# Kernel optimization log

Hardware: AMD Instinct MI355X
Metric: run time of the kernel (lower is better)

The kernel has to match this reference:

```python
import jax, jax.numpy as jnp
import numpy as np

N, B, T, D = 6, 4, 1024, 768
P = 3            # number of prior phases
H, Dh = 2, 32    # n_heads, head_dim
I = H * Dh       # inner_dim
EPS = 1e-5


def setup_inputs() -> dict:
    key = jax.random.key(0)
    ks = jax.random.split(key, 9)
    current_states = jax.random.normal(ks[0], (N, B, T, D), dtype=jnp.float32)
    history_states = jax.random.normal(ks[1], (P, N, B, T, D), dtype=jnp.float32)
    attention_mask = jax.random.randint(ks[2], (B, T), 0, 2, dtype=jnp.int32)
    # Linear weights stored as [in, out] (transposed nn.Linear weight)
    s = 1.0 / np.sqrt(D)
    Wq = jax.random.uniform(ks[3], (N, D, I), jnp.float32, -s, s)  # per-domain q proj
    Wk = jax.random.uniform(ks[4], (D, I), jnp.float32, -s, s)     # shared k proj
    Wv = jax.random.uniform(ks[5], (D, I), jnp.float32, -s, s)     # shared v proj
    so = 1.0 / np.sqrt(I)
    Wo = jax.random.uniform(ks[6], (N, I, D), jnp.float32, -so, so)  # per-domain out proj
    gamma = jnp.ones((N, D), jnp.float32)   # per-domain LayerNorm weight
    beta = jnp.zeros((N, D), jnp.float32)   # per-domain LayerNorm bias
    return {"current_states": current_states, "history_states": history_states,
            "attention_mask": attention_mask, "Wq": Wq, "Wk": Wk, "Wv": Wv,
            "Wo": Wo, "gamma": gamma, "beta": beta}


def reference(current_states, history_states, attention_mask, Wq, Wk, Wv, Wo, gamma, beta):
    x = current_states                                   # [N,B,T,D]
    # concat prior phases along time per domain: [N,B,P*T,D]
    prior = jnp.transpose(history_states, (1, 2, 0, 3, 4)).reshape(N, B, P * T, D)

    q = jnp.einsum('nbtd,ndi->nbti', x, Wq).reshape(N, B, T, H, Dh).transpose(0, 1, 3, 2, 4)       # [N,B,H,T,Dh]
    k = jnp.einsum('nbsd,di->nbsi', prior, Wk).reshape(N, B, P * T, H, Dh).transpose(0, 1, 3, 2, 4)  # [N,B,H,S,Dh]
    v = jnp.einsum('nbsd,di->nbsi', prior, Wv).reshape(N, B, P * T, H, Dh).transpose(0, 1, 3, 2, 4)

    scale = 1.0 / jnp.sqrt(jnp.float32(Dh))
    scores = jnp.einsum('nbhtd,nbhsd->nbhts', q, k) * scale  # [N,B,H,T,P*T]
    full_mask = jnp.tile(attention_mask.astype(jnp.float32), (1, P))  # [B,P*T]
    bias = (1.0 - full_mask)[None, :, None, None, :] * -10000.0
    attn = jax.nn.softmax(scores + bias, axis=-1)
    o = jnp.einsum('nbhts,nbhsd->nbhtd', attn, v)            # [N,B,H,T,Dh]
    o = o.transpose(0, 1, 3, 2, 4).reshape(N, B, T, I)       # [N,B,T,I]
    o = jnp.einsum('nbti,nid->nbtd', o, Wo)                  # [N,B,T,D]

    y = x + o  # residual (dropout p=0)
    mu = jnp.mean(y, axis=-1, keepdims=True)
    var = jnp.mean(jnp.square(y - mu), axis=-1, keepdims=True)
    out = (y - mu) * jax.lax.rsqrt(var + EPS)
    out = out * gamma[:, None, None, :] + beta[:, None, None, :]
    return out
```

## Files before the change

### kernel.cpp

```cpp
#include <hip/hip_runtime.h>
#include <hip/hip_bf16.h>
#include <math.h>

#define NDOM 6
#define BB 4
#define TT 1024
#define DD 768
#define PP 3
#define HH 2
#define DHH 32
#define II 64
#define SS (PP*TT)
#define NROW (NDOM*BB*TT)
#define NKVROW (NDOM*BB*SS)
#define NSPLIT 4
#define NKVB (NKVROW/128)
#define NQB  (NROW/128)
#define LNEPS 1e-5f

typedef unsigned int uint;
typedef uint  u32x4  __attribute__((ext_vector_type(4)));
typedef int   i32x2  __attribute__((ext_vector_type(2)));
typedef float f32x2  __attribute__((ext_vector_type(2)));
typedef float f32x4  __attribute__((ext_vector_type(4)));
typedef float f32x16 __attribute__((ext_vector_type(16)));
typedef __bf16 bf16x8 __attribute__((ext_vector_type(8)));

__device__ __forceinline__ f32x16 mfma32(u32x4 a, u32x4 b, f32x16 c) {
  return __builtin_amdgcn_mfma_f32_32x32x16_bf16(
      __builtin_bit_cast(bf16x8, a), __builtin_bit_cast(bf16x8, b), c, 0, 0, 0);
}

__device__ __forceinline__ uint pkbf(float a, float b) {
  union { __bf16 h[2]; uint u; } v;
  v.h[0] = (__bf16)a; v.h[1] = (__bf16)b;
  return v.u;
}
__device__ __forceinline__ float b2f(uint u16) {
  union { uint i; float f; } v; v.i = u16 << 16; return v.f;
}

__device__ __forceinline__ void plswap(uint a, uint b, uint& x, uint& y) {
#if __has_builtin(__builtin_amdgcn_permlane32_swap)
  i32x2 r = __builtin_amdgcn_permlane32_swap((int)a, (int)b, false, false);
  x = (uint)r.x; y = (uint)r.y;
#else
  uint sa = __shfl_xor(a, 32), sb = __shfl_xor(b, 32);
  bool h1 = (threadIdx.x & 32) != 0;
  x = h1 ? sb : a;
  y = h1 ? b : sa;
#endif
}

__global__ __launch_bounds__(256) void prep_kernel(
    const int* __restrict__ mask, const float* __restrict__ Wk,
    const float* __restrict__ Wv, const float* __restrict__ Wq,
    const float* __restrict__ Wo,
    __hip_bfloat16* __restrict__ Bkv, __hip_bfloat16* __restrict__ Bq,
    __hip_bfloat16* __restrict__ Bo, float* __restrict__ bias2)
{
  int i = blockIdx.x * 256 + threadIdx.x;
  const int N1 = 128 * 768;
  const int N2 = NDOM * 64 * 768;
  const int N3 = NDOM * 768 * 64;
  if (i < N1) {
    int c = i / 768, k = i % 768;
    float v = (c < 64) ? Wk[k * 64 + c] : Wv[k * 64 + (c - 64)];
    Bkv[i] = __float2bfloat16(v);
  } else if (i < N1 + N2) {
    int j = i - N1;
    int n = j / (64 * 768);
    int rem = j % (64 * 768);
    int c = rem / 768, k = rem % 768;
    Bq[j] = __float2bfloat16(Wq[((size_t)n * 768 + k) * 64 + c]);
  } else if (i < N1 + N2 + N3) {
    int j = i - N1 - N2;
    int n = j / (768 * 64);
    int rem = j % (768 * 64);
    int d = rem / 64, k = rem % 64;
    Bo[j] = __float2bfloat16(Wo[((size_t)n * 64 + k) * 768 + d]);
  } else if (i < N1 + N2 + N3 + BB * SS) {
    int j = i - N1 - N2 - N3;
    int b = j / SS, s = j % SS;
    bias2[j] = (1.0f - (float)mask[b * TT + (s & (TT - 1))]) * (-14426.950408889634f);
  }
}

__global__ __launch_bounds__(256) void qkv_gemm_kernel(
    const float* __restrict__ x, const float* __restrict__ hist,
    const __hip_bfloat16* __restrict__ Bkv, const __hip_bfloat16* __restrict__ Bq,
    __hip_bfloat16* __restrict__ Qo, __hip_bfloat16* __restrict__ Kh,
    __hip_bfloat16* __restrict__ Vt2)
{
  __shared__ uint As[2][128 * 32];
  const int tid = threadIdx.x;
  const int lane = tid & 63, w = tid >> 6;
  const int cl = lane & 31, hi = lane >> 5;
  const int r0 = tid >> 3, oct = tid & 7;

  const bool isKV = blockIdx.x < NKVB;
  const float* Asrc;
  int nb = 0, s0 = 0, n = 0, brow = 0;
  if (isKV) {
    brow = blockIdx.x * 128;
    nb = brow / SS; n = nb >> 2;
    int b = nb & 3;
    s0 = brow % SS;
    int p = s0 / TT, t0 = s0 % TT;
    Asrc = hist + (((size_t)(p * NDOM + n) * BB + b) * TT + t0) * 768;
  } else {
    brow = (blockIdx.x - NKVB) * 128;
    n = brow >> 12;
    Asrc = x + (size_t)brow * 768;
  }

  float4 a0[4], a1[4];
  auto ldA = [&](int kk) {
#pragma unroll
    for (int g = 0; g < 4; ++g) {
      const float* ap = Asrc + (size_t)(r0 + 32 * g) * 768 + kk * 64 + oct * 8;
      a0[g] = *(const float4*)ap;
      a1[g] = *(const float4*)(ap + 4);
    }
  };
  auto stA = [&](uint* dst) {
#pragma unroll
    for (int g = 0; g < 4; ++g) {
      int row = r0 + 32 * g;
      u32x4 pk = {pkbf(a0[g].x, a0[g].y), pkbf(a0[g].z, a0[g].w),
                  pkbf(a1[g].x, a1[g].y), pkbf(a1[g].z, a1[g].w)};
      *(u32x4*)&dst[row * 32 + ((oct ^ (row & 7)) << 2)] = pk;
    }
  };

  if (isKV) {
    f32x16 acc0 = {}, acc1 = {}, acc2 = {}, acc3 = {};
    ldA(0);
    for (int kk = 0; kk < 12; ++kk) {
      uint* dst = As[kk & 1];
      stA(dst);
      __syncthreads();
      if (kk + 1 < 12) ldA(kk + 1);
#pragma unroll
      for (int ks = 0; ks < 4; ++ks) {
        int kg = kk * 64 + ks * 16 + hi * 8;
        u32x4 b0 = *(const u32x4*)(Bkv + (size_t)(cl)      * 768 + kg);
        u32x4 b1 = *(const u32x4*)(Bkv + (size_t)(32 + cl) * 768 + kg);
        u32x4 b2 = *(const u32x4*)(Bkv + (size_t)(64 + cl) * 768 + kg);
        u32x4 b3 = *(const u32x4*)(Bkv + (size_t)(96 + cl) * 768 + kg);
        int ro = w * 32 + cl;
        int oc = ks * 2 + hi;
        u32x4 a = *(const u32x4*)&dst[ro * 32 + ((oc ^ (ro & 7)) << 2)];
        acc0 = mfma32(a, b0, acc0);
        acc1 = mfma32(a, b1, acc1);
        acc2 = mfma32(a, b2, acc2);
        acc3 = mfma32(a, b3, acc3);
      }
    }
    {
      const size_t base0 = (size_t)(nb * 2 + 0) * SS;
      const size_t base1 = (size_t)(nb * 2 + 1) * SS;
#pragma unroll
      for (int r = 0; r < 16; ++r) {
        int rl = (r & 3) + 8 * (r >> 2) + 4 * hi;
        int s  = s0 + w * 32 + rl;
        Kh[(base0 + s) * 32 + cl] = __float2bfloat16(acc0[r]);
        Kh[(base1 + s) * 32 + cl] = __float2bfloat16(acc1[r]);
      }
    }
#pragma unroll
    for (int k = 0; k < 4; ++k) {
      int sb = (s0 + w * 32 + 8 * k) >> 3;
      size_t A0 = (((size_t)(nb * 2 + 0) * (SS / 8) + sb) * 32 + cl) * 8 + 4 * hi;
      size_t A1 = (((size_t)(nb * 2 + 1) * (SS / 8) + sb) * 32 + cl) * 8 + 4 * hi;
      *(uint2*)(Vt2 + A0) = uint2{pkbf(acc2[4*k], acc2[4*k+1]), pkbf(acc2[4*k+2], acc2[4*k+3])};
      *(uint2*)(Vt2 + A1) = uint2{pkbf(acc3[4*k], acc3[4*k+1]), pkbf(acc3[4*k+2], acc3[4*k+3])};
    }
  } else {
    const __hip_bfloat16* Bn = Bq + (size_t)n * 64 * 768;
    f32x16 acc0 = {}, acc1 = {};
    ldA(0);
    for (int kk = 0; kk < 12; ++kk) {
      uint* dst = As[kk & 1];
      stA(dst);
      __syncthreads();
      if (kk + 1 < 12) ldA(kk + 1);
#pragma unroll
      for (int ks = 0; ks < 4; ++ks) {
        int kg = kk * 64 + ks * 16 + hi * 8;
        u32x4 b0 = *(const u32x4*)(Bn + (size_t)(cl)      * 768 + kg);
        u32x4 b1 = *(const u32x4*)(Bn + (size_t)(32 + cl) * 768 + kg);
        int ro = w * 32 + cl;
        int oc = ks * 2 + hi;
        u32x4 a = *(const u32x4*)&dst[ro * 32 + ((oc ^ (ro & 7)) << 2)];
        acc0 = mfma32(a, b0, acc0);
        acc1 = mfma32(a, b1, acc1);
      }
    }
#pragma unroll
    for (int r = 0; r < 16; ++r) {
      int rl = (r & 3) + 8 * (r >> 2) + 4 * hi;
      size_t rb = (size_t)(brow + w * 32 + rl) * 64;
      Qo[rb + cl]      = __float2bfloat16(acc0[r]);
      Qo[rb + 32 + cl] = __float2bfloat16(acc1[r]);
    }
  }
}

struct KV { u32x4 k0, k1, k2, k3, v0, v1, v2, v3; };

__global__ __launch_bounds__(256) void attn_kernel(
    const __hip_bfloat16* __restrict__ Q, const __hip_bfloat16* __restrict__ Kh,
    const __hip_bfloat16* __restrict__ Vt2, const float* __restrict__ bias2,
    __hip_bfloat16* __restrict__ Op, float* __restrict__ Mp, float* __restrict__ Lp)
{
  const int tid = threadIdx.x;
  const int lane = tid & 63, w = tid >> 6;
  const int cl = lane & 31, hi = lane >> 5;
  const int bid = blockIdx.x;
  const int g = bid % 48;
  const int rest = bid / 48;
  const int sp = rest >> 3;
  const int tq = rest & 7;
  const int qtile = tq * 4 + w;
  const int h = g & 1, nb = g >> 1;
  const int b = nb & 3;
  const int qrow = nb * TT + qtile * 32;
  const int sbase = sp * (SS / NSPLIT);

  const __hip_bfloat16* Qp = Q + (size_t)(qrow + cl) * 64 + h * 32 + hi * 8;
  u32x4 qf0 = *(const u32x4*)Qp;
  u32x4 qf1 = *(const u32x4*)(Qp + 16);

  const __hip_bfloat16* Kp = Kh + ((size_t)(nb * 2 + h) * SS + sbase) * 32;
  const __hip_bfloat16* Vp = Vt2 + (size_t)(nb * 2 + h) * SS * 32 + (size_t)sbase * 32;
  const float* Bp = bias2 + b * SS + sbase + hi * 4;

  const float scale2 = 0.17677669529663687f * 1.4426950408889634f;
  const f32x2 sc2 = {scale2, scale2};

  f32x16 ot = {};
  float m = -1e30f, lsum = 0.f;

  auto loadKV = [&](int it) {
    KV t;
    const __hip_bfloat16* kp = Kp + (size_t)it * 64 * 32;
    t.k0 = *(const u32x4*)(kp + cl * 32 + hi * 8);
    t.k1 = *(const u32x4*)(kp + cl * 32 + 16 + hi * 8);
    t.k2 = *(const u32x4*)(kp + 1024 + cl * 32 + hi * 8);
    t.k3 = *(const u32x4*)(kp + 1024 + cl * 32 + 16 + hi * 8);
    const __hip_bfloat16* vp = Vp + (size_t)it * 64 * 32;
    t.v0 = *(const u32x4*)(vp + ((0 * 2 + hi) * 32 + cl) * 8);
    t.v1 = *(const u32x4*)(vp + ((1 * 2 + hi) * 32 + cl) * 8);
    t.v2 = *(const u32x4*)(vp + ((2 * 2 + hi) * 32 + cl) * 8);
    t.v3 = *(const u32x4*)(vp + ((3 * 2 + hi) * 32 + cl) * 8);
    return t;
  };

  auto compute = [&](const KV& t, int it) {
    f32x16 pz0 = {}, pz1 = {};
    pz0 = mfma32(t.k0, qf0, pz0);
    pz0 = mfma32(t.k1, qf1, pz0);
    pz1 = mfma32(t.k2, qf0, pz1);
    pz1 = mfma32(t.k3, qf1, pz1);
    const float* bp = Bp + it * 64;
    f32x4 b4[8];
#pragma unroll
    for (int q = 0; q < 8; ++q) b4[q] = *(const f32x4*)(bp + 8 * q);
    f32x2 p2[16];
#pragma unroll
    for (int i = 0; i < 8; ++i) {
      f32x4 bq0 = b4[i >> 1];
      f32x4 bq1 = b4[4 + (i >> 1)];
      f32x2 bv0 = (i & 1) ? f32x2{bq0.z, bq0.w} : f32x2{bq0.x, bq0.y};
      f32x2 bv1 = (i & 1) ? f32x2{bq1.z, bq1.w} : f32x2{bq1.x, bq1.y};
      p2[i]     = f32x2{pz0[2*i], pz0[2*i+1]} * sc2 + bv0;
      p2[8 + i] = f32x2{pz1[2*i], pz1[2*i+1]} * sc2 + bv1;
    }
    f32x2 mx = p2[0];
#pragma unroll
    for (int i = 1; i < 16; ++i) {
      mx.x = fmaxf(mx.x, p2[i].x);
      mx.y = fmaxf(mx.y, p2[i].y);
    }
    float tm = fmaxf(mx.x, mx.y);
    tm = fmaxf(tm, __shfl_xor(tm, 32));
    if (!__all(tm - m <= 8.f)) {
      float mn = fmaxf(m, tm);
      float f = exp2f(m - mn);
#pragma unroll
      for (int i = 0; i < 16; ++i) ot[i] *= f;
      lsum *= f;
      m = mn;
    }
    const f32x2 m2 = {m, m};
    f32x2 s2 = {0.f, 0.f};
#pragma unroll
    for (int i = 0; i < 16; ++i) {
      f32x2 d = p2[i] - m2;
      f32x2 e = {exp2f(d.x), exp2f(d.y)};
      p2[i] = e;
      s2 += e;
    }
    float ts = s2.x + s2.y;
    ts += __shfl_xor(ts, 32);
    lsum += ts;
    uint cv[16];
#pragma unroll
    for (int i = 0; i < 16; ++i) cv[i] = pkbf(p2[i].x, p2[i].y);
    u32x4 pf0, pf1, pf2, pf3;
    {
      uint x0, y0, x1, y1;
      plswap(cv[0], cv[2],  x0, y0); plswap(cv[1], cv[3],  x1, y1);
      pf0 = u32x4{x0, x1, y0, y1};
      plswap(cv[4], cv[6],  x0, y0); plswap(cv[5], cv[7],  x1, y1);
      pf1 = u32x4{x0, x1, y0, y1};
      plswap(cv[8], cv[10], x0, y0); plswap(cv[9], cv[11], x1, y1);
      pf2 = u32x4{x0, x1, y0, y1};
      plswap(cv[12], cv[14], x0, y0); plswap(cv[13], cv[15], x1, y1);
      pf3 = u32x4{x0, x1, y0, y1};
    }
    ot = mfma32(t.v0, pf0, ot);
    ot = mfma32(t.v1, pf1, ot);
    ot = mfma32(t.v2, pf2, ot);
    ot = mfma32(t.v3, pf3, ot);
  };

  KV cur = loadKV(0);
#pragma unroll 1
  for (int it = 0; it < 12; ++it) {
    KV nxt = loadKV(it + 1 < 12 ? it + 1 : 11);
    compute(cur, it);
    cur = nxt;
    __builtin_amdgcn_s_barrier();
  }

  __hip_bfloat16* op = Op + ((size_t)sp * NROW + qrow + cl) * 64 + h * 32 + 4 * hi;
#pragma unroll
  for (int k = 0; k < 4; ++k) {
    uint2 wv = {pkbf(ot[4*k], ot[4*k+1]), pkbf(ot[4*k+2], ot[4*k+3])};
    *(uint2*)(op + 8 * k) = wv;
  }
  if (lane < 32) {
    int mi = ((sp * 24 + nb) * 2 + h) * TT + qtile * 32 + cl;
    Mp[mi] = m;
    Lp[mi] = lsum;
  }
}

__global__ __launch_bounds__(256) void oproj_ln_kernel(
    const float* __restrict__ x, const __hip_bfloat16* __restrict__ Op,
    const float* __restrict__ Mp, const float* __restrict__ Lp,
    const __hip_bfloat16* __restrict__ Bo, const float* __restrict__ gamma,
    const float* __restrict__ beta, float* __restrict__ out)
{
  __shared__ float red[4][32][2];
  __shared__ float redf[32][2];
  const int tid = threadIdx.x;
  const int lane = tid & 63, w = tid >> 6;
  const int cl = lane & 31, hi = lane >> 5;
  const int row0 = blockIdx.x * 32;
  const int n = row0 >> 12;
  const int nb = row0 >> 10;
  const int trow = (row0 & 1023) + cl;
  const int MLS = 24 * 2 * TT;

  float wsp[2][NSPLIT];
#pragma unroll
  for (int h = 0; h < 2; ++h) {
    int mi = (nb * 2 + h) * TT + trow;
    float mv[NSPLIT], lv[NSPLIT];
#pragma unroll
    for (int sp = 0; sp < NSPLIT; ++sp) { mv[sp] = Mp[mi + sp * MLS]; lv[sp] = Lp[mi + sp * MLS]; }
    float ms = mv[0];
#pragma unroll
    for (int sp = 1; sp < NSPLIT; ++sp) ms = fmaxf(ms, mv[sp]);
    float den = 0.f;
#pragma unroll
    for (int sp = 0; sp < NSPLIT; ++sp) { wsp[h][sp] = exp2f(mv[sp] - ms); den = fmaf(lv[sp], wsp[h][sp], den); }
    float inv = 1.0f / den;
#pragma unroll
    for (int sp = 0; sp < NSPLIT; ++sp) wsp[h][sp] *= inv;
  }

  u32x4 af[4];
#pragma unroll
  for (int ks = 0; ks < 4; ++ks) {
    int h = ks >> 1;
    size_t off = (size_t)(row0 + cl) * 64 + ks * 16 + hi * 8;
    f32x2 s0 = {}, s1 = {}, s2 = {}, s3 = {};
#pragma unroll
    for (int sp = 0; sp < NSPLIT; ++sp) {
      u32x4 v = *(const u32x4*)(Op + (size_t)sp * NROW * 64 + off);
      float wv = wsp[h][sp];
      s0 += f32x2{b2f(v[0] & 0xffffu), b2f(v[0] >> 16)} * wv;
      s1 += f32x2{b2f(v[1] & 0xffffu), b2f(v[1] >> 16)} * wv;
      s2 += f32x2{b2f(v[2] & 0xffffu), b2f(v[2] >> 16)} * wv;
      s3 += f32x2{b2f(v[3] & 0xffffu), b2f(v[3] >> 16)} * wv;
    }
    af[ks] = u32x4{pkbf(s0.x, s0.y), pkbf(s1.x, s1.y), pkbf(s2.x, s2.y), pkbf(s3.x, s3.y)};
  }

  const __hip_bfloat16* Bp = Bo + ((size_t)n * 768 + w * 192 + cl) * 64 + hi * 8;
  f32x16 acc[6] = {};
#pragma unroll
  for (int ks = 0; ks < 4; ++ks) {
#pragma unroll
    for (int t = 0; t < 6; ++t) {
      u32x4 bb = *(const u32x4*)(Bp + (size_t)(t * 32) * 64 + ks * 16);
      acc[t] = mfma32(af[ks], bb, acc[t]);
    }
  }

  float s1[16], s2[16];
#pragma unroll
  for (int r = 0; r < 16; ++r) { s1[r] = 0.f; s2[r] = 0.f; }
#pragma unroll
  for (int t = 0; t < 6; ++t) {
#pragma unroll
    for (int r = 0; r < 16; ++r) {
      int R = (r & 3) + 8 * (r >> 2) + 4 * hi;
      int col = w * 192 + t * 32 + cl;
      float y = acc[t][r] + x[(size_t)(row0 + R) * 768 + col];
      acc[t][r] = y;
      s1[r] += y;
      s2[r] = fmaf(y, y, s2[r]);
    }
  }
#pragma unroll
  for (int r = 0; r < 16; ++r) {
#pragma unroll
    for (int off = 1; off < 32; off <<= 1) {
      s1[r] += __shfl_xor(s1[r], off);
      s2[r] += __shfl_xor(s2[r], off);
    }
  }
  if (cl == 0) {
#pragma unroll
    for (int r = 0; r < 16; ++r) {
      int R = (r & 3) + 8 * (r >> 2) + 4 * hi;
      red[w][R][0] = s1[r];
      red[w][R][1] = s2[r];
    }
  }
  __syncthreads();
  if (tid < 64) {
    int R = tid & 31, st = tid >> 5;
    redf[R][st] = red[0][R][st] + red[1][R][st] + red[2][R][st] + red[3][R][st];
  }
  __syncthreads();

  float gv[6], bv[6];
#pragma unroll
  for (int t = 0; t < 6; ++t) {
    int col = w * 192 + t * 32 + cl;
    gv[t] = gamma[n * 768 + col];
    bv[t] = beta[n * 768 + col];
  }
#pragma unroll
  for (int r = 0; r < 16; ++r) {
    int R = (r & 3) + 8 * (r >> 2) + 4 * hi;
    float mu = redf[R][0] * (1.0f / 768.0f);
    float var = redf[R][1] * (1.0f / 768.0f) - mu * mu;
    float rs = rsqrtf(var + LNEPS);
#pragma unroll
    for (int t = 0; t < 6; ++t) {
      int col = w * 192 + t * 32 + cl;
      out[(size_t)(row0 + R) * 768 + col] = (acc[t][r] - mu) * rs * gv[t] + bv[t];
    }
  }
}

extern "C" void kernel_launch(void* const* d_in, const int* in_sizes, int n_in,
                              void* d_out, int out_size, void* d_ws, size_t ws_size,
                              hipStream_t stream) {
  const float* x     = (const float*)d_in[0];
  const float* hist  = (const float*)d_in[1];
  const int*   mask  = (const int*)d_in[2];
  const float* Wq    = (const float*)d_in[3];
  const float* Wk    = (const float*)d_in[4];
  const float* Wv    = (const float*)d_in[5];
  const float* Wo    = (const float*)d_in[6];
  const float* gamma = (const float*)d_in[7];
  const float* beta  = (const float*)d_in[8];
  float* out = (float*)d_out;

  char* ws = (char*)d_ws;
  __hip_bfloat16* Qb  = (__hip_bfloat16*)ws;  ws += (size_t)NROW * II * 2;
  __hip_bfloat16* Kh  = (__hip_bfloat16*)ws;  ws += (size_t)NKVROW * II * 2;
  __hip_bfloat16* Vt2 = (__hip_bfloat16*)ws;  ws += (size_t)NKVROW * II * 2;
  __hip_bfloat16* Op  = (__hip_bfloat16*)ws;  ws += (size_t)NSPLIT * NROW * II * 2;
  float* Mp           = (float*)ws;           ws += (size_t)NSPLIT * 24 * 2 * TT * 4;
  float* Lp           = (float*)ws;           ws += (size_t)NSPLIT * 24 * 2 * TT * 4;
  __hip_bfloat16* Bkv = (__hip_bfloat16*)ws;  ws += (size_t)128 * 768 * 2;
  __hip_bfloat16* Bq  = (__hip_bfloat16*)ws;  ws += (size_t)NDOM * 64 * 768 * 2;
  __hip_bfloat16* Bo  = (__hip_bfloat16*)ws;  ws += (size_t)NDOM * 768 * 64 * 2;
  float* bias2        = (float*)ws;           ws += (size_t)BB * SS * 4;

  const int PREP_N = 128*768 + NDOM*64*768 + NDOM*768*64 + BB*SS;
  prep_kernel<<<(PREP_N + 255) / 256, 256, 0, stream>>>(mask, Wk, Wv, Wq, Wo, Bkv, Bq, Bo, bias2);
  qkv_gemm_kernel<<<NKVB + NQB, 256, 0, stream>>>(x, hist, Bkv, Bq, Qb, Kh, Vt2);
  attn_kernel<<<48 * 8 * NSPLIT, 256, 0, stream>>>(Qb, Kh, Vt2, bias2, Op, Mp, Lp);
  oproj_ln_kernel<<<NROW / 32, 256, 0, stream>>>(x, Op, Mp, Lp, Bo, gamma, beta, out);
}
```

Measured before the change: 228.6 us.

## Restructure QKV GEMM with async global-to-LDS triple buffering and smaller tiles

```diff
diff --git a/kernel.cpp b/kernel.cpp
--- a/kernel.cpp
+++ b/kernel.cpp
@@ -14,8 +14,8 @@
 #define NROW (NDOM*BB*TT)
 #define NKVROW (NDOM*BB*SS)
 #define NSPLIT 4
-#define NKVB (NKVROW/128)
-#define NQB  (NROW/128)
+#define NKVB (NKVROW/64)
+#define NQB  (NROW/64)
 #define LNEPS 1e-5f
 
 typedef unsigned int uint;
@@ -51,6 +51,17 @@
   y = h1 ? b : sa;
 #endif
 }
+
+#if __has_builtin(__builtin_amdgcn_global_load_lds)
+#define HAS_GLL 1
+typedef __attribute__((address_space(3))) uint lds_u32;
+typedef __attribute__((address_space(1))) uint glb_u32;
+__device__ __forceinline__ void gload_lds16(const float* src, float* lds_base) {
+  __builtin_amdgcn_global_load_lds((const glb_u32*)src, (lds_u32*)lds_base, 16, 0, 0);
+}
+#else
+#define HAS_GLL 0
+#endif
 
 __global__ __launch_bounds__(256) void prep_kernel(
     const int* __restrict__ mask, const float* __restrict__ Wk,
@@ -86,123 +97,120 @@
   }
 }
 
-__global__ __launch_bounds__(256) void qkv_gemm_kernel(
+__global__ __launch_bounds__(256, 3) void qkv_gemm_kernel(
     const float* __restrict__ x, const float* __restrict__ hist,
     const __hip_bfloat16* __restrict__ Bkv, const __hip_bfloat16* __restrict__ Bq,
     __hip_bfloat16* __restrict__ Qo, __hip_bfloat16* __restrict__ Kh,
     __hip_bfloat16* __restrict__ Vt2)
 {
-  __shared__ uint As[2][128 * 32];
+  __shared__ float As[3][64 * 64];
   const int tid = threadIdx.x;
   const int lane = tid & 63, w = tid >> 6;
   const int cl = lane & 31, hi = lane >> 5;
-  const int r0 = tid >> 3, oct = tid & 7;
+  const int wr = w >> 1, wc = w & 1;
 
   const bool isKV = blockIdx.x < NKVB;
   const float* Asrc;
   int nb = 0, s0 = 0, n = 0, brow = 0;
   if (isKV) {
-    brow = blockIdx.x * 128;
+    brow = blockIdx.x * 64;
     nb = brow / SS; n = nb >> 2;
     int b = nb & 3;
     s0 = brow % SS;
     int p = s0 / TT, t0 = s0 % TT;
     Asrc = hist + (((size_t)(p * NDOM + n) * BB + b) * TT + t0) * 768;
   } else {
-    brow = (blockIdx.x - NKVB) * 128;
+    brow = (blockIdx.x - NKVB) * 64;
     n = brow >> 12;
     Asrc = x + (size_t)brow * 768;
   }
-
-  float4 a0[4], a1[4];
-  auto ldA = [&](int kk) {
-#pragma unroll
-    for (int g = 0; g < 4; ++g) {
-      const float* ap = Asrc + (size_t)(r0 + 32 * g) * 768 + kk * 64 + oct * 8;
-      a0[g] = *(const float4*)ap;
-      a1[g] = *(const float4*)(ap + 4);
+  const __hip_bfloat16* Bb0 = isKV ? (Bkv + (size_t)(wc * 64 + cl) * 768)
+                                   : (Bq + (size_t)n * 64 * 768 + (size_t)(wc * 32 + cl) * 768);
+  const __hip_bfloat16* Bb1 = Bkv + (size_t)(wc * 64 + 32 + cl) * 768;
+
+  auto stage = [&](int kk, int buf) {
+#pragma unroll
+    for (int j = 0; j < 4; ++j) {
+      int row = w * 16 + j * 4 + (lane >> 4);
+      int gs = (lane & 15) ^ (row & 15);
+      const float* src = Asrc + (size_t)row * 768 + kk * 64 + gs * 4;
+#if HAS_GLL
+      gload_lds16(src, &As[buf][(w * 16 + j * 4) * 64]);
+#else
+      f32x4 v = *(const f32x4*)src;
+      *(f32x4*)(&As[buf][(w * 16 + j * 4) * 64] + lane * 4) = v;
+#endif
     }
   };
-  auto stA = [&](uint* dst) {
-#pragma unroll
-    for (int g = 0; g < 4; ++g) {
-      int row = r0 + 32 * g;
-      u32x4 pk = {pkbf(a0[g].x, a0[g].y), pkbf(a0[g].z, a0[g].w),
-                  pkbf(a1[g].x, a1[g].y), pkbf(a1[g].z, a1[g].w)};
-      *(u32x4*)&dst[row * 32 + ((oct ^ (row & 7)) << 2)] = pk;
+
+  u32x4 breg[8];
+  auto loadB = [&](int kk) {
+#pragma unroll
+    for (int ks = 0; ks < 4; ++ks) {
+      int kg = kk * 64 + ks * 16 + hi * 8;
+      breg[ks] = *(const u32x4*)(Bb0 + kg);
+      if (isKV) breg[4 + ks] = *(const u32x4*)(Bb1 + kg);
     }
   };
 
+  f32x16 acc0 = {}, acc1 = {};
+
+  stage(0, 0);
+  stage(1, 1);
+  loadB(0);
+  stage(2, 2);
+
+#pragma unroll
+  for (int kk = 0; kk < 12; ++kk) {
+    if (kk <= 9) { asm volatile("s_waitcnt vmcnt(4)" ::: "memory"); }
+    else         { asm volatile("s_waitcnt vmcnt(0)" ::: "memory"); }
+    __builtin_amdgcn_s_barrier();
+    {
+      const int buf = kk % 3;
+      const int row = wr * 32 + cl;
+#pragma unroll
+      for (int ks = 0; ks < 4; ++ks) {
+        int t = ks * 4 + hi * 2;
+        int sA = (t ^ (row & 15)) * 4;
+        int sB = ((t + 1) ^ (row & 15)) * 4;
+        f32x4 a0 = *(const f32x4*)&As[buf][row * 64 + sA];
+        f32x4 a1 = *(const f32x4*)&As[buf][row * 64 + sB];
+        u32x4 a = {pkbf(a0.x, a0.y), pkbf(a0.z, a0.w), pkbf(a1.x, a1.y), pkbf(a1.z, a1.w)};
+        acc0 = mfma32(a, breg[ks], acc0);
+        if (isKV) acc1 = mfma32(a, breg[4 + ks], acc1);
+      }
+    }
+    __builtin_amdgcn_s_barrier();
+    if (kk + 1 < 12) loadB(kk + 1);
+    if (kk + 3 < 12) stage(kk + 3, kk % 3);
+  }
+
   if (isKV) {
-    f32x16 acc0 = {}, acc1 = {}, acc2 = {}, acc3 = {};
-    ldA(0);
-    for (int kk = 0; kk < 12; ++kk) {
-      uint* dst = As[kk & 1];
-      stA(dst);
-      __syncthreads();
-      if (kk + 1 < 12) ldA(kk + 1);
-#pragma unroll
-      for (int ks = 0; ks < 4; ++ks) {
-        int kg = kk * 64 + ks * 16 + hi * 8;
-        u32x4 b0 = *(const u32x4*)(Bkv + (size_t)(cl)      * 768 + kg);
-        u32x4 b1 = *(const u32x4*)(Bkv + (size_t)(32 + cl) * 768 + kg);
-        u32x4 b2 = *(const u32x4*)(Bkv + (size_t)(64 + cl) * 768 + kg);
-        u32x4 b3 = *(const u32x4*)(Bkv + (size_t)(96 + cl) * 768 + kg);
-        int ro = w * 32 + cl;
-        int oc = ks * 2 + hi;
-        u32x4 a = *(const u32x4*)&dst[ro * 32 + ((oc ^ (ro & 7)) << 2)];
-        acc0 = mfma32(a, b0, acc0);
-        acc1 = mfma32(a, b1, acc1);
-        acc2 = mfma32(a, b2, acc2);
-        acc3 = mfma32(a, b3, acc3);
-      }
-    }
-    {
+    if (wc == 0) {
       const size_t base0 = (size_t)(nb * 2 + 0) * SS;
       const size_t base1 = (size_t)(nb * 2 + 1) * SS;
 #pragma unroll
       for (int r = 0; r < 16; ++r) {
         int rl = (r & 3) + 8 * (r >> 2) + 4 * hi;
-        int s  = s0 + w * 32 + rl;
+        int s  = s0 + wr * 32 + rl;
         Kh[(base0 + s) * 32 + cl] = __float2bfloat16(acc0[r]);
         Kh[(base1 + s) * 32 + cl] = __float2bfloat16(acc1[r]);
       }
-    }
-#pragma unroll
-    for (int k = 0; k < 4; ++k) {
-      int sb = (s0 + w * 32 + 8 * k) >> 3;
-      size_t A0 = (((size_t)(nb * 2 + 0) * (SS / 8) + sb) * 32 + cl) * 8 + 4 * hi;
-      size_t A1 = (((size_t)(nb * 2 + 1) * (SS / 8) + sb) * 32 + cl) * 8 + 4 * hi;
-      *(uint2*)(Vt2 + A0) = uint2{pkbf(acc2[4*k], acc2[4*k+1]), pkbf(acc2[4*k+2], acc2[4*k+3])};
-      *(uint2*)(Vt2 + A1) = uint2{pkbf(acc3[4*k], acc3[4*k+1]), pkbf(acc3[4*k+2], acc3[4*k+3])};
+    } else {
+#pragma unroll
+      for (int k = 0; k < 4; ++k) {
+        int sb = (s0 + wr * 32 + 8 * k) >> 3;
+        size_t A0 = (((size_t)(nb * 2 + 0) * (SS / 8) + sb) * 32 + cl) * 8 + 4 * hi;
+        size_t A1 = (((size_t)(nb * 2 + 1) * (SS / 8) + sb) * 32 + cl) * 8 + 4 * hi;
+        *(uint2*)(Vt2 + A0) = uint2{pkbf(acc0[4*k], acc0[4*k+1]), pkbf(acc0[4*k+2], acc0[4*k+3])};
+        *(uint2*)(Vt2 + A1) = uint2{pkbf(acc1[4*k], acc1[4*k+1]), pkbf(acc1[4*k+2], acc1[4*k+3])};
+      }
     }
   } else {
-    const __hip_bfloat16* Bn = Bq + (size_t)n * 64 * 768;
-    f32x16 acc0 = {}, acc1 = {};
-    ldA(0);
-    for (int kk = 0; kk < 12; ++kk) {
-      uint* dst = As[kk & 1];
-      stA(dst);
-      __syncthreads();
-      if (kk + 1 < 12) ldA(kk + 1);
-#pragma unroll
-      for (int ks = 0; ks < 4; ++ks) {
-        int kg = kk * 64 + ks * 16 + hi * 8;
-        u32x4 b0 = *(const u32x4*)(Bn + (size_t)(cl)      * 768 + kg);
-        u32x4 b1 = *(const u32x4*)(Bn + (size_t)(32 + cl) * 768 + kg);
-        int ro = w * 32 + cl;
-        int oc = ks * 2 + hi;
-        u32x4 a = *(const u32x4*)&dst[ro * 32 + ((oc ^ (ro & 7)) << 2)];
-        acc0 = mfma32(a, b0, acc0);
-        acc1 = mfma32(a, b1, acc1);
-      }
-    }
 #pragma unroll
     for (int r = 0; r < 16; ++r) {
       int rl = (r & 3) + 8 * (r >> 2) + 4 * hi;
-      size_t rb = (size_t)(brow + w * 32 + rl) * 64;
-      Qo[rb + cl]      = __float2bfloat16(acc0[r]);
-      Qo[rb + 32 + cl] = __float2bfloat16(acc1[r]);
+      Qo[(size_t)(brow + wr * 32 + rl) * 64 + wc * 32 + cl] = __float2bfloat16(acc0[r]);
     }
   }
 }
```

Measured after the change: 228.8 us. About the same (+0.1%).
